# Performance work log

Measured on AMD Instinct MI355X. Metric: run time of the kernel, lower is better.

Reference implementation:

```python
import jax, jax.numpy as jnp
from jax import lax
import numpy as np

WIN = 9
WIN_SIZE = WIN * WIN
EPS = float(np.exp(-15.0))  # np.power(np.e, -15)


def box_sum(x, win=WIN):
    """Depthwise box-sum with SAME padding, done separably (H then W).
    x: [B, C, H, W] -> [B, C, H, W]."""
    C = x.shape[1]
    pad = win // 2
    kh = jnp.ones((C, 1, win, 1), x.dtype)
    kw = jnp.ones((C, 1, 1, win), x.dtype)
    x = lax.conv_general_dilated(x, kh, (1, 1), [(pad, pad), (0, 0)],
                                 feature_group_count=C)
    x = lax.conv_general_dilated(x, kw, (1, 1), [(0, 0), (pad, pad)],
                                 feature_group_count=C)
    return x


def setup_inputs() -> dict:
    key = jax.random.key(0)
    k1, k2 = jax.random.split(key)
    B, C, H, W = 16, 1, 768, 768
    I = jax.random.uniform(k1, (B, C, H, W), dtype=jnp.float32)
    J = jax.random.uniform(k2, (B, C, H, W), dtype=jnp.float32)
    return {"I": I, "J": J}


def reference(I, J):
    # stack the 5 moment channels: I, J, I^2, J^2, I*J
    tmp = jnp.concatenate([I, J, I * I, J * J, I * J], axis=1)  # [B,5,H,W]
    tmp = box_sum(tmp)
    I_sum, J_sum = tmp[:, 0:1], tmp[:, 1:2]
    I2_sum, J2_sum, IJ_sum = tmp[:, 2:3], tmp[:, 3:4], tmp[:, 4:5]

    win_size = jnp.float32(WIN_SIZE)
    u_I = I_sum / win_size
    u_J = J_sum / win_size

    cross = IJ_sum - (u_J * I_sum + u_I * J_sum) + u_I * u_J * win_size
    I_var = I2_sum - 2.0 * u_I * I_sum + u_I * u_I * win_size
    J_var = J2_sum - 2.0 * u_J * J_sum + u_J * u_J * win_size

    nz = (I_var * J_var) > EPS
    cross = jnp.where(nz, cross, 1.0)
    I_var = jnp.where(nz, I_var, 1.0)
    J_var = jnp.where(nz, J_var, 1.0)

    cc = cross * cross / (I_var * J_var + EPS)
    return -1.0 * jnp.mean(cc, axis=(1, 2, 3)) + 1.0  # [B]
```

## Files before the change

### kernel.cpp

```cpp
#include <hip/hip_runtime.h>


constexpr int BATCH = 16;
constexpr int H = 768;
constexpr int W = 768;
constexpr float INV_WS = 1.0f / 81.0f;
constexpr float EPS = 3.0590232050182579e-07f;

constexpr int SEG = 12;
constexpr int NSEG = H / SEG;
constexpr int BANDW = 248;
constexpr int NTHREADS = 256;

#define F4ADD(a, u)    { a.x += u.x; a.y += u.y; a.z += u.z; a.w += u.w; }
#define F4SUB(a, u)    { a.x -= u.x; a.y -= u.y; a.z -= u.z; a.w -= u.w; }
#define F4FMA(a, u, v) { a.x = fmaf(u.x, v.x, a.x); a.y = fmaf(u.y, v.y, a.y); \
                         a.z = fmaf(u.z, v.z, a.z); a.w = fmaf(u.w, v.w, a.w); }
#define F4FMS(a, u, v) { a.x = fmaf(u.x, -v.x, a.x); a.y = fmaf(u.y, -v.y, a.y); \
                         a.z = fmaf(u.z, -v.z, a.z); a.w = fmaf(u.w, -v.w, a.w); }

#define HSUM_SHFL(c, h)                                                   \
    {                                                                     \
        const float s3 = c.w;                                             \
        const float s2 = c.w + c.z;                                       \
        const float s1 = s2 + c.y;                                        \
        const float s0 = s1 + c.x;                         \
        const float p1 = c.x + c.y;                                      \
        const float p2 = p1 + c.z;                                        \
        const float pn = __shfl_down(s0, 1, 64);                          \
        const float q0 = __shfl_down(c.x, 2, 64);                         \
        const float q1 = __shfl_down(p1, 2, 64);                          \
        const float q2 = __shfl_down(p2, 2, 64);                          \
        const float q3 = __shfl_down(s0, 2, 64);                          \
        h[0] = s0 + pn + q0;                                              \
        h[1] = s1 + pn + q1;                                              \
        h[2] = s2 + pn + q2;                                              \
        h[3] = s3 + pn + q3;                                              \
    }

#define LD2(NI, NJ, rbase)                                                \
    {                                                                     \
        _Pragma("unroll")                                                 \
        for (int k = 0; k < 2; ++k) {                                     \
            const int rr = (rbase) + k;                                   \
            const int rc = min(max(rr, 0), H - 1);                        \
            const float mk = (rr >= 0 && rr < H) ? fm : 0.0f;             \
            float4 ti = *(const float4*)(Ib + (size_t)rc * W + ca);       \
            float4 tj = *(const float4*)(Jb + (size_t)rc * W + ca);       \
            ti.x *= mk; ti.y *= mk; ti.z *= mk; ti.w *= mk;               \
            tj.x *= mk; tj.y *= mk; tj.z *= mk; tj.w *= mk;               \
            NI[k] = ti; NJ[k] = tj;                                       \
        }                                                                 \
    }

#define CHUNK(VI, VJ, OI, OJ)                                             \
    _Pragma("unroll")                                                     \
    for (int k = 0; k < 2; ++k) {                                         \
        F4ADD(cs0, VI[k]) F4ADD(cs1, VJ[k])                               \
        F4FMA(cs2, VI[k], VI[k]) F4FMA(cs3, VJ[k], VJ[k])                 \
        F4FMA(cs4, VI[k], VJ[k])                                          \
        float hI[4], hJ[4], hII[4], hJJ[4], hIJ[4];                       \
        HSUM_SHFL(cs0, hI)                                                \
        HSUM_SHFL(cs1, hJ)                                                \
        HSUM_SHFL(cs2, hII)                                               \
        HSUM_SHFL(cs3, hJJ)                                               \
        HSUM_SHFL(cs4, hIJ)                                               \
        float rowsum = 0.0f;                                              \
        _Pragma("unroll")                                                 \
        for (int e = 0; e < 4; ++e) {                                     \
            const float u = -hI[e] * INV_WS;                              \
            const float cross = fmaf(u, hJ[e], hIJ[e]);                   \
            const float Ivar  = fmaf(u, hI[e], hII[e]);                   \
            const float Jvar  = fmaf(-hJ[e] * INV_WS, hJ[e], hJJ[e]);     \
            float prod = Ivar * Jvar;                                     \
            float num  = cross * cross;                                   \
            if (!(prod > EPS)) { prod = 1.0f; num = 1.0f; }               \
            float inv_;                                                   \
            asm("v_rcp_f32 %0, %1" : "=v"(inv_) : "v"(prod + EPS));       \
            rowsum = fmaf(num, inv_, rowsum);                             \
        }                                                                 \
        accum += live ? rowsum : 0.0f;                                    \
        F4SUB(cs0, OI[k]) F4SUB(cs1, OJ[k])                               \
        F4FMS(cs2, OI[k], OI[k]) F4FMS(cs3, OJ[k], OJ[k])                 \
        F4FMS(cs4, OI[k], OJ[k])                                          \
    }

__launch_bounds__(NTHREADS, 2)
__global__ void lncc_pipe(const float* __restrict__ gI, const float* __restrict__ gJ,
                          float* __restrict__ part)
{
    __shared__ float wsum[4];

    const int lane = threadIdx.x & 63;
    const int band = threadIdx.x >> 6;
    const int r0   = blockIdx.x * SEG;
    const int b    = blockIdx.y;
    const int c0   = band * BANDW - 4 + 4 * lane;
    const float fm = (c0 >= 0 && c0 + 3 < W) ? 1.0f : 0.0f;
    const int ca   = min(max(c0, 0), W - 4);
    const bool live = (lane <= 61) && (band * BANDW + 4 * lane + 3 < W);

    const float* __restrict__ Ib = gI + (size_t)b * (H * W);
    const float* __restrict__ Jb = gJ + (size_t)b * (H * W);

    float4 cs0 = {0,0,0,0}, cs1 = {0,0,0,0}, cs2 = {0,0,0,0},
           cs3 = {0,0,0,0}, cs4 = {0,0,0,0};

    float4 W0i[2], W0j[2], W1i[2], W1j[2], W2i[2], W2j[2], W3i[2], W3j[2];
    LD2(W0i, W0j, r0 - 4)
    LD2(W1i, W1j, r0 - 2)
    LD2(W2i, W2j, r0)
    LD2(W3i, W3j, r0 + 2)

    float4 I0i[2], I0j[2], I1i[2], I1j[2], I2i[2], I2j[2];
    float4 I3i[2], I3j[2], I4i[2], I4j[2], I5i[2], I5j[2];
    float4 OAi[2], OAj[2], OBi[2], OBj[2];
    LD2(I0i, I0j, r0 + 4)
    LD2(I1i, I1j, r0 + 6)
    LD2(OAi, OAj, r0 - 4)

#define WACC(WI, WJ)                                                      \
    _Pragma("unroll")                                                     \
    for (int k = 0; k < 2; ++k) {                                         \
        F4ADD(cs0, WI[k]) F4ADD(cs1, WJ[k])                               \
        F4FMA(cs2, WI[k], WI[k]) F4FMA(cs3, WJ[k], WJ[k])                 \
        F4FMA(cs4, WI[k], WJ[k])                                          \
    }
    WACC(W0i, W0j) WACC(W1i, W1j) WACC(W2i, W2j) WACC(W3i, W3j)
#undef WACC

    float accum = 0.0f;

    LD2(I2i, I2j, r0 + 8)   LD2(OBi, OBj, r0 - 2)   CHUNK(I0i, I0j, OAi, OAj)
    LD2(I3i, I3j, r0 + 10)  LD2(OAi, OAj, r0)       CHUNK(I1i, I1j, OBi, OBj)
    LD2(I4i, I4j, r0 + 12)  LD2(OBi, OBj, r0 + 2)   CHUNK(I2i, I2j, OAi, OAj)
    LD2(I5i, I5j, r0 + 14)  LD2(OAi, OAj, r0 + 4)   CHUNK(I3i, I3j, OBi, OBj)
                            LD2(OBi, OBj, r0 + 6)   CHUNK(I4i, I4j, OAi, OAj)
                                                    CHUNK(I5i, I5j, OBi, OBj)

    #pragma unroll
    for (int off = 32; off > 0; off >>= 1)
        accum += __shfl_xor(accum, off, 64);
    if (lane == 0) wsum[band] = accum;
    __syncthreads();
    if (threadIdx.x == 0)
        part[blockIdx.y * NSEG + blockIdx.x] = wsum[0] + wsum[1] + wsum[2] + wsum[3];
}

__global__ void finalize2(const float* __restrict__ part, float* __restrict__ out) {
    const int b = threadIdx.y;
    const int x = threadIdx.x;
    float v = part[b * NSEG + x];
    #pragma unroll
    for (int off = 32; off > 0; off >>= 1)
        v += __shfl_xor(v, off, 64);
    if (x == 0)
        out[b] = 1.0f - v * (1.0f / (float)(H * W));
}

extern "C" void kernel_launch(void* const* d_in, const int* in_sizes, int n_in,
                              void* d_out, int out_size, void* d_ws, size_t ws_size,
                              hipStream_t stream) {
    const float* I = (const float*)d_in[0];
    const float* J = (const float*)d_in[1];
    float* out  = (float*)d_out;
    float* part = (float*)d_ws;

    dim3 grid(NSEG, BATCH);
    lncc_pipe<<<grid, NTHREADS, 0, stream>>>(I, J, part);

    finalize2<<<1, dim3(64, BATCH), 0, stream>>>(part, out);
}
```

Before: 36.95 us.

## Pack the mostly idle fourth column band into one warp per eight segments

In the old layout the fourth wavefront of every block covered only the last 24 columns, so most of its lanes did no useful work. Now the first three bands cover columns 0-743. The remaining 28 columns are handled by band 3 of only every eighth block, which splits its lanes across eight row segments. Each wavefront writes its own partial sum directly, which removes the shared-memory reduction and the __syncthreads, and finalize is updated to sum 200 partials per batch. The aim is to cut wasted loads and compute on the edge columns. In exchange it adds divergent early returns and a less coalesced access pattern in the packed warp.

```diff
diff --git a/kernel.cpp b/kernel.cpp
--- a/kernel.cpp
+++ b/kernel.cpp
@@ -11,6 +11,7 @@
 constexpr int NSEG = H / SEG;
 constexpr int BANDW = 248;
 constexpr int NTHREADS = 256;
+constexpr int PPI = 200;
 
 #define F4ADD(a, u)    { a.x += u.x; a.y += u.y; a.z += u.z; a.w += u.w; }
 #define F4SUB(a, u)    { a.x -= u.x; a.y -= u.y; a.z -= u.z; a.w -= u.w; }
@@ -25,7 +26,7 @@
         const float s2 = c.w + c.z;                                       \
         const float s1 = s2 + c.y;                                        \
         const float s0 = s1 + c.x;                         \
-        const float p1 = c.x + c.y;                                      \
+        const float p1 = c.x + c.y;                                       \
         const float p2 = p1 + c.z;                                        \
         const float pn = __shfl_down(s0, 1, 64);                          \
         const float q0 = __shfl_down(c.x, 2, 64);                         \
@@ -86,19 +87,30 @@
     }
 
 __launch_bounds__(NTHREADS, 2)
-__global__ void lncc_pipe(const float* __restrict__ gI, const float* __restrict__ gJ,
+__global__ void lncc_pack(const float* __restrict__ gI, const float* __restrict__ gJ,
                           float* __restrict__ part)
 {
-    __shared__ float wsum[4];
-
     const int lane = threadIdx.x & 63;
     const int band = threadIdx.x >> 6;
-    const int r0   = blockIdx.x * SEG;
+    const int seg  = blockIdx.x;
     const int b    = blockIdx.y;
-    const int c0   = band * BANDW - 4 + 4 * lane;
+
+    int r0, c0;
+    bool live;
+    if (band < 3) {
+        r0 = seg * SEG;
+        c0 = band * BANDW - 4 + 4 * lane;
+        live = (lane <= 61);
+    } else {
+        if (seg & 7) return;
+        const int rch = lane >> 3;
+        const int cg  = lane & 7;
+        r0 = (seg + rch) * SEG;
+        c0 = 740 + 4 * cg;
+        live = (cg <= 5);
+    }
     const float fm = (c0 >= 0 && c0 + 3 < W) ? 1.0f : 0.0f;
     const int ca   = min(max(c0, 0), W - 4);
-    const bool live = (lane <= 61) && (band * BANDW + 4 * lane + 3 < W);
 
     const float* __restrict__ Ib = gI + (size_t)b * (H * W);
     const float* __restrict__ Jb = gJ + (size_t)b * (H * W);
@@ -141,16 +153,20 @@
     #pragma unroll
     for (int off = 32; off > 0; off >>= 1)
         accum += __shfl_xor(accum, off, 64);
-    if (lane == 0) wsum[band] = accum;
-    __syncthreads();
-    if (threadIdx.x == 0)
-        part[blockIdx.y * NSEG + blockIdx.x] = wsum[0] + wsum[1] + wsum[2] + wsum[3];
+    if (lane == 0) {
+        if (band < 3)
+            part[b * PPI + seg * 3 + band] = accum;
+        else
+            part[b * PPI + 192 + (seg >> 3)] = accum;
+    }
 }
 
 __global__ void finalize2(const float* __restrict__ part, float* __restrict__ out) {
     const int b = threadIdx.y;
     const int x = threadIdx.x;
-    float v = part[b * NSEG + x];
+    const int base = b * PPI;
+    float v = part[base + x] + part[base + 64 + x] + part[base + 128 + x];
+    if (x < 8) v += part[base + 192 + x];
     #pragma unroll
     for (int off = 32; off > 0; off >>= 1)
         v += __shfl_xor(v, off, 64);
@@ -167,7 +183,7 @@
     float* part = (float*)d_ws;
 
     dim3 grid(NSEG, BATCH);
-    lncc_pipe<<<grid, NTHREADS, 0, stream>>>(I, J, part);
+    lncc_pack<<<grid, NTHREADS, 0, stream>>>(I, J, part);
 
     finalize2<<<1, dim3(64, BATCH), 0, stream>>>(part, out);
 }
```

New measurement: 35.94 us. -2.7%, faster.
